# Performance work log

Measured on AMD Instinct MI355X. Metric: run time of the kernel, lower is better.

## Reference

```python
import jax, jax.numpy as jnp
import numpy as np

B, F_IN, D_IN = 1024, 64, 64
N_CAPS, D_CAPS = 32, 64
ROUTINGS = 3
HEADS = 2
EPS = 1e-7  # K.epsilon()


def setup_inputs() -> dict:
    key = jax.random.key(0)
    ks = jax.random.split(key, 8)
    P = N_CAPS * (N_CAPS - 1) // 2
    return {
        "x": jax.random.normal(ks[0], (B, F_IN, D_IN), jnp.float32),
        "reweight_W": jax.random.normal(ks[1], (D_IN, N_CAPS, D_CAPS), jnp.float32) * 0.05,
        "routing_init": 10.0 * jax.random.truncated_normal(ks[2], -2.0, 2.0, (N_CAPS, F_IN), jnp.float32),
        "kernel_fm": jnp.full((N_CAPS, 1), 0.5, jnp.float32),
        "bias_fm": jnp.zeros((D_CAPS,), jnp.float32),
        "kernel_mf": jnp.ones((P, 1), jnp.float32),
        "bias_mf": jnp.zeros((D_CAPS,), jnp.float32),
        "kernel_highint": jnp.full((N_CAPS, 1), 0.5, jnp.float32),
        "bias_highint": jnp.zeros((D_CAPS * HEADS,), jnp.float32),
        "W_query": jax.random.normal(ks[3], (D_CAPS, D_CAPS * HEADS), jnp.float32) * 0.05,
        "W_key": jax.random.normal(ks[4], (D_CAPS, D_CAPS * HEADS), jnp.float32) * 0.05,
        "W_value": jax.random.normal(ks[5], (D_CAPS, D_CAPS * HEADS), jnp.float32) * 0.05,
        "W_res": jax.random.normal(ks[6], (D_CAPS, D_CAPS * HEADS), jnp.float32) * 0.05,
    }


def _squash(v):
    s = jnp.sum(v * v, axis=-1, keepdims=True) + EPS
    return (jnp.sqrt(s) / (0.5 + s)) * v


def _heads(t):
    # [B,N,H*F] -> [H,B,N,F] (matches tf.stack(tf.split(t, H, axis=2)))
    b, n, _ = t.shape
    return t.reshape(b, n, HEADS, D_CAPS).transpose(2, 0, 1, 3)


def reference(x, reweight_W, routing_init, kernel_fm, bias_fm, kernel_mf, bias_mf,
              kernel_highint, bias_highint, W_query, W_key, W_value, W_res):
    # inputs_hat: [B, N, F, C]
    inputs_hat = jnp.einsum('bfd,dnc->bnfc', x, reweight_W)
    b_logits = jnp.broadcast_to(routing_init[None], (x.shape[0], N_CAPS, F_IN))
    for _ in range(ROUTINGS):
        c = jax.nn.softmax(b_logits, axis=1)            # softmax over capsules
        outputs = _squash(jnp.einsum('bnf,bnfc->bnc', c, inputs_hat))
        b_logits = b_logits + jnp.einsum('bnc,bnfc->bnf', outputs, inputs_hat)
    c = jax.nn.softmax(b_logits, axis=1)
    routing_score = c[..., None]                        # [B,N,F,1]
    attention_output = routing_score * inputs_hat       # [B,N,F,C]

    # FM per-field: square-of-sum minus sum-of-square over input capsules
    sum_f = jnp.sum(attention_output, axis=2)           # [B,N,C]
    field_fm = sum_f ** 2 - jnp.sum(attention_output ** 2, axis=2)
    hi_fm = jnp.sum(field_fm * kernel_fm[None], axis=1) + bias_fm  # [B,C]

    field_wise_vectors = sum_f                          # [B,N,C]

    # pairwise MF interactions (itertools.combinations order == triu indices)
    li, ri = np.triu_indices(N_CAPS, k=1)
    emb_prod = field_wise_vectors[:, li] * field_wise_vectors[:, ri]  # [B,P,C]
    h_mf = jnp.sum(emb_prod * kernel_mf[None], axis=1) + bias_mf      # [B,C]

    # InteractingLayer (multi-head self-attention over fields, use_res=True)
    q = _heads(jnp.einsum('bnd,de->bne', field_wise_vectors, W_query))  # [H,B,N,F]
    k = _heads(jnp.einsum('bnd,de->bne', field_wise_vectors, W_key))
    v = _heads(jnp.einsum('bnd,de->bne', field_wise_vectors, W_value))
    attn = jax.nn.softmax(jnp.einsum('hbnf,hbmf->hbnm', q, k), axis=-1)
    out = jnp.einsum('hbnm,hbmf->hbnf', attn, v)        # [H,B,N,F]
    out = out.transpose(1, 2, 0, 3).reshape(x.shape[0], N_CAPS, HEADS * D_CAPS)
    res = jnp.einsum('bnd,de->bne', field_wise_vectors, W_res)
    fv2 = jax.nn.relu(out + res)                        # [B,N,H*F]
    high_int = jnp.sum(fv2 * kernel_highint[None], axis=1) + bias_highint  # [B,2C]

    return jnp.concatenate([hi_fm, h_mf, high_int], axis=-1), routing_score
```

## Files before the change

### kernel.cpp

```cpp
#include <hip/hip_runtime.h>


#define EPS_SQ 1e-7f

typedef __attribute__((ext_vector_type(8))) short bf16x8;
typedef __attribute__((ext_vector_type(4))) float floatx4;

__device__ __forceinline__ int lidx(int r, int c) {
  return r * 68 + ((((c >> 2) ^ (r >> 2)) & 15) << 2) + (c & 3);
}
__device__ __forceinline__ int lidx64(int r, int c) {
  return r * 64 + ((((c >> 2) ^ r ^ (r >> 2)) & 15) << 2) + (c & 3);
}
__device__ __forceinline__ unsigned short f2bf(float f) {
  unsigned u = __float_as_uint(f);
  u += 0x7FFFu + ((u >> 16) & 1u);
  return (unsigned short)(u >> 16);
}

__global__ __launch_bounds__(256) void k_prep2(
    const float* __restrict__ W, const float* __restrict__ Wq,
    const float* __restrict__ Wk, const float* __restrict__ kmf,
    float* __restrict__ Qb, float* __restrict__ Ab, float* __restrict__ Kb,
    unsigned short* __restrict__ Wbf)
{
  const int t = threadIdx.x;
  if (blockIdx.x < 32) {
    __shared__ __align__(16) float Mn[64 * 68];
    const int n = blockIdx.x;
#pragma unroll
    for (int k = 0; k < 4; k++) {
      int lin = t + 256 * k; int d = lin >> 4; int c0 = (lin & 15) << 2;
      *(float4*)&Mn[lidx(d, c0)] = *(const float4*)(W + d * 2048 + n * 64 + c0);
    }
    __syncthreads();
    const int d1 = (t >> 4) * 4, d2 = (t & 15) * 4;
    float acc[4][4] = {};
    for (int cq = 0; cq < 64; cq += 4) {
      float m1[4][4], m2[4][4];
#pragma unroll
      for (int i = 0; i < 4; i++) *(float4*)m1[i] = *(const float4*)&Mn[lidx(d1 + i, cq)];
#pragma unroll
      for (int j = 0; j < 4; j++) *(float4*)m2[j] = *(const float4*)&Mn[lidx(d2 + j, cq)];
#pragma unroll
      for (int i = 0; i < 4; i++)
#pragma unroll
        for (int j = 0; j < 4; j++) {
          float s = 0.f;
#pragma unroll
          for (int k = 0; k < 4; k++) s += m1[i][k] * m2[j][k];
          acc[i][j] += s;
        }
    }
#pragma unroll
    for (int i = 0; i < 4; i++)
      *(float4*)(Qb + n * 4096 + (d1 + i) * 64 + d2) = *(float4*)acc[i];
  } else if (blockIdx.x < 40) {
    __shared__ __align__(16) float wkS[64 * 68];
    __shared__ __align__(16) float wqS[16 * 68];
    const int hb = blockIdx.x - 32;
    const int h = hb & 1, rg = hb >> 1;
#pragma unroll
    for (int k = 0; k < 4; k++) {
      int lin = t + 256 * k; int dp = lin >> 4; int e0 = (lin & 15) << 2;
      *(float4*)&wkS[lidx(dp, e0)] = *(const float4*)(Wk + dp * 128 + h * 64 + e0);
    }
    {
      int dl = t >> 4, e0 = (t & 15) << 2;
      *(float4*)&wqS[lidx(dl, e0)] = *(const float4*)(Wq + (rg * 16 + dl) * 128 + h * 64 + e0);
    }
    __syncthreads();
    const int dl = t >> 4, dp0 = (t & 15) << 2;
    float acc[4] = {};
    for (int e = 0; e < 64; e += 4) {
      float q4[4];
      *(float4*)q4 = *(const float4*)&wqS[lidx(dl, e)];
#pragma unroll
      for (int c = 0; c < 4; c++) {
        float mr[4];
        *(float4*)mr = *(const float4*)&wkS[lidx(dp0 + c, e)];
        acc[c] += q4[0] * mr[0] + q4[1] * mr[1] + q4[2] * mr[2] + q4[3] * mr[3];
      }
    }
    *(float4*)(Ab + h * 4096 + (rg * 16 + dl) * 64 + dp0) = *(float4*)acc;
  } else if (blockIdx.x == 40) {
    __shared__ float Ks[1024];
    *(float4*)&Ks[t * 4] = make_float4(0.f, 0.f, 0.f, 0.f);
    __syncthreads();
    if (t < 248) {
#pragma unroll
      for (int j = 0; j < 2; j++) {
        int p = t * 2 + j;
        if (p < 496) {
          int l = 0, rem = p;
          while (rem >= 31 - l) { rem -= 31 - l; ++l; }
          int r = l + 1 + rem;
          float v = kmf[p];
          Ks[l * 32 + r] = v;
          Ks[r * 32 + l] = v;
        }
      }
    }
    __syncthreads();
    *(float4*)&Kb[t * 4] = *(const float4*)&Ks[t * 4];
  } else {
    const int n = blockIdx.x - 41;
#pragma unroll
    for (int k = 0; k < 2; k++) {
      int lin = t + 256 * k;
      int c = lin >> 3, dg = lin & 7;
      unsigned short tmp[8];
#pragma unroll
      for (int dl = 0; dl < 8; dl++)
        tmp[dl] = f2bf(W[(dg * 8 + dl) * 2048 + n * 64 + c]);
      *(uint4*)&Wbf[n * 4096 + c * 64 + ((dg ^ (c & 7)) << 3)] = *(uint4*)tmp;
    }
  }
}

__global__ __launch_bounds__(512, 4) void k_route3(
    const float* __restrict__ x, const float* __restrict__ W,
    const float* __restrict__ rinit, const float* __restrict__ Qb,
    float* __restrict__ rs, float* __restrict__ fwv)
{
  __shared__ __align__(16) float smem[2 * 10240];

  const int t = threadIdx.x;
  const int tb = t >> 8, tt = t & 255;
  const int b = blockIdx.x * 2 + tb;

  float* xs  = smem + tb * 10240;
  float* bS  = smem + tb * 10240 + 4096;
  float* cOw = smem + tb * 10240 + 6144;
  float* xcS = smem + tb * 10240 + 8192;

  float* xc0 = smem + 8192;
  float* xc1 = smem + 10240 + 8192;
  float* ow0 = smem + 6144;
  float* ow1 = smem + 10240 + 6144;

#pragma unroll
  for (int k = 0; k < 4; k++) {
    int lin = tt + 256 * k; int f = lin >> 4; int d0 = (lin & 15) << 2;
    *(float4*)&xs[lidx64(f, d0)] = *(const float4*)(x + b * 4096 + f * 64 + d0);
  }
#pragma unroll
  for (int k = 0; k < 2; k++) {
    int lin = tt + 256 * k; int n = lin >> 4; int f0 = (lin & 15) << 2;
    *(float4*)&bS[lidx64(n, f0)] = *(const float4*)(rinit + n * 64 + f0);
  }
  __syncthreads();

  const int tn = tt >> 4, tlo = tt & 15;
  const int nq = t >> 4, sub = t & 15;

  for (int it = 0; it < 4; it++) {
    {
      const int nl = tt & 31, fg = tt >> 5;
#pragma unroll
      for (int qq = 0; qq < 2; qq++) {
        const int f0 = (fg * 2 + qq) * 4;
        float v[4];
        *(float4*)v = *(const float4*)&bS[lidx64(nl, f0)];
        float e[4];
#pragma unroll
        for (int j = 0; j < 4; j++) {
          float m = v[j];
          m = fmaxf(m, __shfl_xor(m, 16, 64));
          m = fmaxf(m, __shfl_xor(m, 8, 64));
          m = fmaxf(m, __shfl_xor(m, 4, 64));
          m = fmaxf(m, __shfl_xor(m, 2, 64));
          m = fmaxf(m, __shfl_xor(m, 1, 64));
          e[j] = __expf(v[j] - m);
          float s = e[j];
          s += __shfl_xor(s, 16, 64);
          s += __shfl_xor(s, 8, 64);
          s += __shfl_xor(s, 4, 64);
          s += __shfl_xor(s, 2, 64);
          s += __shfl_xor(s, 1, 64);
          e[j] /= s;
        }
        *(float4*)&cOw[lidx64(nl, f0)] = *(float4*)e;
      }
    }
    __syncthreads();
    if (it == 3) {
#pragma unroll
      for (int k = 0; k < 2; k++) {
        int lin = tt + 256 * k;
        int n = lin >> 4, fq = lin & 15;
        float4 v = *(const float4*)&cOw[lidx64(n, fq * 4)];
        *(float4*)(rs + b * 2048 + n * 64 + fq * 4) = v;
      }
    }
    {
      const int n0 = tn * 2, d0 = tlo * 4;
      float acc[2][4] = {{0, 0, 0, 0}, {0, 0, 0, 0}};
      for (int fq = 0; fq < 16; fq++) {
        float c0[4], c1[4];
        *(float4*)c0 = *(const float4*)&cOw[lidx64(n0, fq * 4)];
        *(float4*)c1 = *(const float4*)&cOw[lidx64(n0 + 1, fq * 4)];
#pragma unroll
        for (int j = 0; j < 4; j++) {
          float xr[4];
          *(float4*)xr = *(const float4*)&xs[lidx64(fq * 4 + j, d0)];
#pragma unroll
          for (int i = 0; i < 4; i++) {
            acc[0][i] += c0[j] * xr[i];
            acc[1][i] += c1[j] * xr[i];
          }
        }
      }
      *(float4*)&xcS[lidx64(n0, d0)] = *(float4*)acc[0];
      *(float4*)&xcS[lidx64(n0 + 1, d0)] = *(float4*)acc[1];
    }
    __syncthreads();
    if (it == 3) break;

    {
      const float* Qn = Qb + nq * 4096 + sub * 4;
      float y0[4] = {}, y1[4] = {};
#pragma unroll 4
      for (int dq = 0; dq < 16; dq++) {
        float xv0[4], xv1[4];
        *(float4*)xv0 = *(const float4*)&xc0[lidx64(nq, dq * 4)];
        *(float4*)xv1 = *(const float4*)&xc1[lidx64(nq, dq * 4)];
#pragma unroll
        for (int j = 0; j < 4; j++) {
          float4 q = *(const float4*)(Qn + (dq * 4 + j) * 64);
          y0[0] += xv0[j] * q.x; y0[1] += xv0[j] * q.y;
          y0[2] += xv0[j] * q.z; y0[3] += xv0[j] * q.w;
          y1[0] += xv1[j] * q.x; y1[1] += xv1[j] * q.y;
          y1[2] += xv1[j] * q.z; y1[3] += xv1[j] * q.w;
        }
      }
      float xa0[4], xa1[4];
      *(float4*)xa0 = *(const float4*)&xc0[lidx64(nq, sub * 4)];
      *(float4*)xa1 = *(const float4*)&xc1[lidx64(nq, sub * 4)];
      float ps0 = y0[0] * xa0[0] + y0[1] * xa0[1] + y0[2] * xa0[2] + y0[3] * xa0[3];
      float ps1 = y1[0] * xa1[0] + y1[1] * xa1[1] + y1[2] * xa1[2] + y1[3] * xa1[3];
      ps0 += __shfl_xor(ps0, 1, 64); ps0 += __shfl_xor(ps0, 2, 64);
      ps0 += __shfl_xor(ps0, 4, 64); ps0 += __shfl_xor(ps0, 8, 64);
      ps1 += __shfl_xor(ps1, 1, 64); ps1 += __shfl_xor(ps1, 2, 64);
      ps1 += __shfl_xor(ps1, 4, 64); ps1 += __shfl_xor(ps1, 8, 64);
      const float ss0 = ps0 + EPS_SQ, ss1 = ps1 + EPS_SQ;
      const float sc0 = sqrtf(ss0) / (0.5f + ss0);
      const float sc1 = sqrtf(ss1) / (0.5f + ss1);
      float o0[4] = {y0[0] * sc0, y0[1] * sc0, y0[2] * sc0, y0[3] * sc0};
      float o1[4] = {y1[0] * sc1, y1[1] * sc1, y1[2] * sc1, y1[3] * sc1};
      *(float4*)&ow0[lidx64(nq, sub * 4)] = *(float4*)o0;
      *(float4*)&ow1[lidx64(nq, sub * 4)] = *(float4*)o1;
    }
    __syncthreads();

    {
      const int n0 = tn * 2, f0 = tlo * 4;
      float acc[2][4] = {{0, 0, 0, 0}, {0, 0, 0, 0}};
      for (int dq = 0; dq < 64; dq += 4) {
        float o[2][4];
        *(float4*)o[0] = *(const float4*)&cOw[lidx64(n0, dq)];
        *(float4*)o[1] = *(const float4*)&cOw[lidx64(n0 + 1, dq)];
#pragma unroll
        for (int i = 0; i < 4; i++) {
          float xr[4];
          *(float4*)xr = *(const float4*)&xs[lidx64(f0 + i, dq)];
#pragma unroll
          for (int k = 0; k < 4; k++) {
            acc[0][i] += o[0][k] * xr[k];
            acc[1][i] += o[1][k] * xr[k];
          }
        }
      }
#pragma unroll
      for (int j = 0; j < 2; j++) {
        float tmp[4];
        *(float4*)tmp = *(const float4*)&bS[lidx64(n0 + j, f0)];
#pragma unroll
        for (int i = 0; i < 4; i++) tmp[i] += acc[j][i];
        *(float4*)&bS[lidx64(n0 + j, f0)] = *(float4*)tmp;
      }
    }
    __syncthreads();
  }

  {
    const float* Wn = W + nq * 64 + sub * 4;
    float a0[4] = {}, a1[4] = {};
#pragma unroll 4
    for (int dq = 0; dq < 16; dq++) {
      float xv0[4], xv1[4];
      *(float4*)xv0 = *(const float4*)&xc0[lidx64(nq, dq * 4)];
      *(float4*)xv1 = *(const float4*)&xc1[lidx64(nq, dq * 4)];
#pragma unroll
      for (int j = 0; j < 4; j++) {
        float4 w = *(const float4*)(Wn + (dq * 4 + j) * 2048);
        a0[0] += xv0[j] * w.x; a0[1] += xv0[j] * w.y;
        a0[2] += xv0[j] * w.z; a0[3] += xv0[j] * w.w;
        a1[0] += xv1[j] * w.x; a1[1] += xv1[j] * w.y;
        a1[2] += xv1[j] * w.z; a1[3] += xv1[j] * w.w;
      }
    }
    const int b0g = blockIdx.x * 2;
    *(float4*)(fwv + b0g * 2048 + nq * 64 + sub * 4) = *(float4*)a0;
    *(float4*)(fwv + (b0g + 1) * 2048 + nq * 64 + sub * 4) = *(float4*)a1;
  }
}

__global__ __launch_bounds__(256) void k_ih(
    const float* __restrict__ x, const unsigned short* __restrict__ Wbf,
    const float* __restrict__ rs, float* __restrict__ ssq)
{
  __shared__ __align__(16) unsigned short xB[4 * 64 * 64];
  __shared__ unsigned short cF2[4 * 8 * 64];
  const int n_oct = (blockIdx.x & 3) << 3, b0 = (blockIdx.x >> 2) * 4;
  const int t = threadIdx.x, w = t >> 6, lane = t & 63;

#pragma unroll
  for (int k = 0; k < 16; k++) {
    int ch = t + 256 * k;
    int bb = ch >> 10, rem = ch & 1023;
    int f = rem >> 4, fq = rem & 15;
    int dg = fq >> 1, half = fq & 1;
    float4 v = *(const float4*)(x + ((b0 + bb) * 64 + f) * 64 + fq * 4);
    unsigned p0 = f2bf(v.x) | ((unsigned)f2bf(v.y) << 16);
    unsigned p1 = f2bf(v.z) | ((unsigned)f2bf(v.w) << 16);
    *(uint2*)&xB[bb * 4096 + f * 64 + ((dg ^ (f & 7)) << 3) + half * 4] =
        make_uint2(p0, p1);
  }
#pragma unroll
  for (int nn = 0; nn < 8; nn++) {
    float v = rs[(b0 + w) * 2048 + (n_oct + nn) * 64 + lane];
    cF2[(w * 8 + nn) * 64 + lane] = f2bf(v * v);
  }
  __syncthreads();

  const int m = lane & 15, q = lane >> 4, ms = m & 7;
  bf16x8 a[4][2];
#pragma unroll
  for (int mi = 0; mi < 4; mi++) {
    const unsigned short* bp = xB + w * 4096 + (mi * 16 + m) * 64;
#pragma unroll
    for (int kk = 0; kk < 2; kk++)
      a[mi][kk] = *(const bf16x8*)&bp[((kk * 4 + q) ^ ms) << 3];
  }

  for (int np = 0; np < 4; np++) {
    const int n0 = n_oct + np * 2;
#pragma unroll
    for (int nn = 0; nn < 2; nn++) {
      bf16x8 bf[4][2];
#pragma unroll
      for (int ci = 0; ci < 4; ci++) {
        const unsigned short* bp = Wbf + (n0 + nn) * 4096 + (ci * 16 + m) * 64;
#pragma unroll
        for (int kk = 0; kk < 2; kk++)
          bf[ci][kk] = *(const bf16x8*)&bp[((kk * 4 + q) ^ ms) << 3];
      }
      float ps[4] = {0.f, 0.f, 0.f, 0.f};
      const unsigned short* cf = cF2 + (w * 8 + np * 2 + nn) * 64 + q * 4;
#pragma unroll
      for (int mi = 0; mi < 4; mi++) {
        float cfv[4];
#pragma unroll
        for (int r = 0; r < 4; r++)
          cfv[r] = __uint_as_float((unsigned)cf[mi * 16 + r] << 16);
#pragma unroll
        for (int ci = 0; ci < 4; ci++) {
          floatx4 c0 = {0.f, 0.f, 0.f, 0.f};
          c0 = __builtin_amdgcn_mfma_f32_16x16x32_bf16(a[mi][0], bf[ci][0], c0, 0, 0, 0);
          c0 = __builtin_amdgcn_mfma_f32_16x16x32_bf16(a[mi][1], bf[ci][1], c0, 0, 0, 0);
#pragma unroll
          for (int r = 0; r < 4; r++) { float tv = c0[r]; ps[ci] += cfv[r] * tv * tv; }
        }
      }
#pragma unroll
      for (int ci = 0; ci < 4; ci++) {
        ps[ci] += __shfl_xor(ps[ci], 16, 64);
        ps[ci] += __shfl_xor(ps[ci], 32, 64);
      }
      if (q == 0) {
#pragma unroll
        for (int ci = 0; ci < 4; ci++)
          ssq[(b0 + w) * 2048 + (n0 + nn) * 64 + ci * 16 + m] = ps[ci];
      }
    }
  }
}

__global__ __launch_bounds__(256) void k_attn(
    const float* __restrict__ fwv, const float* __restrict__ ssq,
    const float* __restrict__ Ab, const float* __restrict__ Kb,
    const float* __restrict__ Wv, const float* __restrict__ Wr,
    const float* __restrict__ kfm, const float* __restrict__ bfm,
    const float* __restrict__ bmf, const float* __restrict__ khi,
    const float* __restrict__ bhi, float* __restrict__ out0)
{
  __shared__ __align__(16) float smem[8832];
  float* fwS  = smem;
  float* pS   = smem + 2176;
  float* bufA = smem + 4480;
  float* tS   = smem + 6656;
  float* vS   = smem + 4480;
  float* redH = smem + 2176;
  float* Kf   = smem + 4480;
  float* red1 = smem + 5536;

  const int b = blockIdx.x, t = threadIdx.x;
  const int tn = t >> 4, te = t & 15;
  const int n0 = tn * 2, e0 = te * 8, d0 = te * 4;

#pragma unroll
  for (int k = 0; k < 2; k++) {
    int lin = t + 256 * k; int nn = lin >> 4; int c0 = (lin & 15) << 2;
    *(float4*)&fwS[lidx(nn, c0)] = *(const float4*)(fwv + b * 2048 + nn * 64 + c0);
  }
  __syncthreads();

  for (int h = 0; h < 2; h++) {
    float tacc[2][4] = {};
    for (int half = 0; half < 2; half++) {
#pragma unroll
      for (int k = 0; k < 2; k++) {
        int lin = t + 256 * k; int d = lin >> 4; int c0 = (lin & 15) << 2;
        *(float4*)&bufA[lidx(d, c0)] =
            *(const float4*)(Ab + h * 4096 + (half * 32 + d) * 64 + c0);
      }
      __syncthreads();
      for (int dq = 0; dq < 32; dq += 4) {
        float fw0[4], fw1[4];
        *(float4*)fw0 = *(const float4*)&fwS[lidx(n0, half * 32 + dq)];
        *(float4*)fw1 = *(const float4*)&fwS[lidx(n0 + 1, half * 32 + dq)];
#pragma unroll
        for (int j = 0; j < 4; j++) {
          float mr[4];
          *(float4*)mr = *(const float4*)&bufA[lidx(dq + j, d0)];
#pragma unroll
          for (int c = 0; c < 4; c++) {
            tacc[0][c] += fw0[j] * mr[c];
            tacc[1][c] += fw1[j] * mr[c];
          }
        }
      }
      __syncthreads();
    }
    *(float4*)&tS[lidx(n0, d0)] = *(float4*)tacc[0];
    *(float4*)&tS[lidx(n0 + 1, d0)] = *(float4*)tacc[1];
    __syncthreads();
    {
      const int m0 = te * 2;
      float s00 = 0.f, s01 = 0.f, s10 = 0.f, s11 = 0.f;
      for (int kk = 0; kk < 16; kk++) {
        float ta0[4], ta1[4], f0[4], f1[4];
        *(float4*)ta0 = *(const float4*)&tS[lidx(n0, kk * 4)];
        *(float4*)ta1 = *(const float4*)&tS[lidx(n0 + 1, kk * 4)];
        *(float4*)f0 = *(const float4*)&fwS[lidx(m0, kk * 4)];
        *(float4*)f1 = *(const float4*)&fwS[lidx(m0 + 1, kk * 4)];
#pragma unroll
        for (int j = 0; j < 4; j++) {
          s00 += ta0[j] * f0[j]; s01 += ta0[j] * f1[j];
          s10 += ta1[j] * f0[j]; s11 += ta1[j] * f1[j];
        }
      }
      pS[(h * 32 + n0) * 36 + m0] = s00;
      pS[(h * 32 + n0) * 36 + m0 + 1] = s01;
      pS[(h * 32 + n0 + 1) * 36 + m0] = s10;
      pS[(h * 32 + n0 + 1) * 36 + m0 + 1] = s11;
    }
    __syncthreads();
  }

  {
    const int r = t >> 2, sub = t & 3;
    const int base = r * 36 + sub * 8;
    float v0[4], v1[4];
    *(float4*)v0 = *(const float4*)&pS[base];
    *(float4*)v1 = *(const float4*)&pS[base + 4];
    float mx = fmaxf(fmaxf(fmaxf(v0[0], v0[1]), fmaxf(v0[2], v0[3])),
                     fmaxf(fmaxf(v1[0], v1[1]), fmaxf(v1[2], v1[3])));
    mx = fmaxf(mx, __shfl_xor(mx, 1, 64));
    mx = fmaxf(mx, __shfl_xor(mx, 2, 64));
    float sum = 0.f;
#pragma unroll
    for (int j = 0; j < 4; j++) { v0[j] = __expf(v0[j] - mx); sum += v0[j]; }
#pragma unroll
    for (int j = 0; j < 4; j++) { v1[j] = __expf(v1[j] - mx); sum += v1[j]; }
    sum += __shfl_xor(sum, 1, 64);
    sum += __shfl_xor(sum, 2, 64);
    const float inv = 1.0f / sum;
#pragma unroll
    for (int j = 0; j < 4; j++) { v0[j] *= inv; v1[j] *= inv; }
    *(float4*)&pS[base] = *(float4*)v0;
    *(float4*)&pS[base + 4] = *(float4*)v1;
  }
  __syncthreads();

  {
    float acc[2][8] = {};
    for (int dq = 0; dq < 64; dq += 4) {
      float fw0[4], fw1[4];
      *(float4*)fw0 = *(const float4*)&fwS[lidx(n0, dq)];
      *(float4*)fw1 = *(const float4*)&fwS[lidx(n0 + 1, dq)];
#pragma unroll
      for (int jj = 0; jj < 4; jj++) {
        float w8[8];
        *(float4*)&w8[0] = *(const float4*)(Wv + (dq + jj) * 128 + e0);
        *(float4*)&w8[4] = *(const float4*)(Wv + (dq + jj) * 128 + e0 + 4);
#pragma unroll
        for (int j = 0; j < 8; j++) {
          acc[0][j] += fw0[jj] * w8[j];
          acc[1][j] += fw1[jj] * w8[j];
        }
      }
    }
    *(float4*)&vS[n0 * 132 + e0] = *(float4*)&acc[0][0];
    *(float4*)&vS[n0 * 132 + e0 + 4] = *(float4*)&acc[0][4];
    *(float4*)&vS[(n0 + 1) * 132 + e0] = *(float4*)&acc[1][0];
    *(float4*)&vS[(n0 + 1) * 132 + e0 + 4] = *(float4*)&acc[1][4];
  }
  __syncthreads();

  {
    const int h2 = te >> 3;
    float pacc[2][8] = {};
    for (int m4 = 0; m4 < 8; m4++) {
      float p0v[4], p1v[4];
      *(float4*)p0v = *(const float4*)&pS[(h2 * 32 + n0) * 36 + m4 * 4];
      *(float4*)p1v = *(const float4*)&pS[(h2 * 32 + n0 + 1) * 36 + m4 * 4];
#pragma unroll
      for (int mm = 0; mm < 4; mm++) {
        const int m = m4 * 4 + mm;
        float vr[8];
        *(float4*)&vr[0] = *(const float4*)&vS[m * 132 + e0];
        *(float4*)&vr[4] = *(const float4*)&vS[m * 132 + e0 + 4];
#pragma unroll
        for (int j = 0; j < 8; j++) {
          pacc[0][j] += p0v[mm] * vr[j];
          pacc[1][j] += p1v[mm] * vr[j];
        }
      }
    }
    for (int dq = 0; dq < 64; dq += 4) {
      float fw0[4], fw1[4];
      *(float4*)fw0 = *(const float4*)&fwS[lidx(n0, dq)];
      *(float4*)fw1 = *(const float4*)&fwS[lidx(n0 + 1, dq)];
#pragma unroll
      for (int jj = 0; jj < 4; jj++) {
        float w8[8];
        *(float4*)&w8[0] = *(const float4*)(Wr + (dq + jj) * 128 + e0);
        *(float4*)&w8[4] = *(const float4*)(Wr + (dq + jj) * 128 + e0 + 4);
#pragma unroll
        for (int j = 0; j < 8; j++) {
          pacc[0][j] += fw0[jj] * w8[j];
          pacc[1][j] += fw1[jj] * w8[j];
        }
      }
    }
    __syncthreads();
    {
      float kh0 = khi[n0], kh1 = khi[n0 + 1];
      float ph[8];
#pragma unroll
      for (int j = 0; j < 8; j++)
        ph[j] = kh0 * fmaxf(pacc[0][j], 0.f) + kh1 * fmaxf(pacc[1][j], 0.f);
      *(float4*)&redH[tn * 132 + e0] = *(float4*)&ph[0];
      *(float4*)&redH[tn * 132 + e0 + 4] = *(float4*)&ph[4];
    }
  }
  {
    const int p4 = t * 4;
    float4 kv = *(const float4*)(Kb + p4);
    const int n = p4 >> 5, r = p4 & 31;
    Kf[n * 33 + r]     = kv.x;
    Kf[n * 33 + r + 1] = kv.y;
    Kf[n * 33 + r + 2] = kv.z;
    Kf[n * 33 + r + 3] = kv.w;
  }
  __syncthreads();

  {
    float acc[2][4] = {{0, 0, 0, 0}, {0, 0, 0, 0}};
    for (int r = 0; r < 32; r++) {
      const float k0 = Kf[n0 * 33 + r];
      const float k1 = Kf[(n0 + 1) * 33 + r];
      float fr[4];
      *(float4*)fr = *(const float4*)&fwS[lidx(r, d0)];
#pragma unroll
      for (int i = 0; i < 4; i++) {
        acc[0][i] += k0 * fr[i];
        acc[1][i] += k1 * fr[i];
      }
    }
    *(float4*)&tS[lidx(n0, d0)] = *(float4*)acc[0];
    *(float4*)&tS[lidx(n0 + 1, d0)] = *(float4*)acc[1];
  }
  __syncthreads();

  if (t < 128) {
    float s = 0.f;
#pragma unroll
    for (int k = 0; k < 16; k++) s += redH[k * 132 + t];
    out0[b * 256 + 128 + t] = s + bhi[t];
  }
  {
    const int c = t & 63, nq = t >> 6;
    float p = 0.f;
#pragma unroll
    for (int k = 0; k < 8; k++) {
      int nn = nq * 8 + k;
      float fv = fwS[lidx(nn, c)];
      float sv = ssq[b * 2048 + nn * 64 + c];
      p += (fv * fv - sv) * kfm[nn];
    }
    red1[nq * 68 + c] = p;
    float hmf = 0.f;
#pragma unroll
    for (int l8 = 0; l8 < 8; l8++) {
      const int l = nq * 8 + l8;
      hmf += fwS[lidx(l, c)] * tS[lidx(l, c)];
    }
    red1[(4 + nq) * 68 + c] = hmf;
  }
  __syncthreads();
  if (t < 64) {
    out0[b * 256 + t] = red1[t] + red1[68 + t] + red1[136 + t] + red1[204 + t] + bfm[t];
    float h2 = red1[272 + t] + red1[340 + t] + red1[408 + t] + red1[476 + t];
    out0[b * 256 + 64 + t] = 0.5f * h2 + bmf[t];
  }
}

extern "C" void kernel_launch(void* const* d_in, const int* in_sizes, int n_in,
                              void* d_out, int out_size, void* d_ws, size_t ws_size,
                              hipStream_t stream) {
  (void)in_sizes; (void)n_in; (void)out_size; (void)ws_size;
  const float* x     = (const float*)d_in[0];
  const float* W     = (const float*)d_in[1];
  const float* rinit = (const float*)d_in[2];
  const float* kfm   = (const float*)d_in[3];
  const float* bfm   = (const float*)d_in[4];
  const float* kmf   = (const float*)d_in[5];
  const float* bmf   = (const float*)d_in[6];
  const float* khi   = (const float*)d_in[7];
  const float* bhi   = (const float*)d_in[8];
  const float* Wq    = (const float*)d_in[9];
  const float* Wk    = (const float*)d_in[10];
  const float* Wv    = (const float*)d_in[11];
  const float* Wr    = (const float*)d_in[12];

  float* out0 = (float*)d_out;
  float* rs   = out0 + 1024 * 256;

  float* ws   = (float*)d_ws;
  float* Abuf = ws;
  float* Kbuf = ws + 8192;
  float* Qbuf = ws + 16384;
  unsigned short* Wbf = (unsigned short*)(ws + 262144);
  float* fwv  = ws + 2097152;
  float* ssq  = ws + 2 * 2097152;

  k_prep2<<<73, 256, 0, stream>>>(W, Wq, Wk, kmf, Qbuf, Abuf, Kbuf, Wbf);
  k_route3<<<512, 512, 0, stream>>>(x, W, rinit, Qbuf, rs, fwv);
  k_ih<<<1024, 256, 0, stream>>>(x, Wbf, rs, ssq);
  k_attn<<<1024, 256, 0, stream>>>(fwv, ssq, Abuf, Kbuf, Wv, Wr,
                                   kfm, bfm, bmf, khi, bhi, out0);
}
```

Baseline: 252.2 us.

## Fuse squared-sum MFMA kernel into attention kernel, drop ssq buffer

```diff
diff --git a/kernel.cpp b/kernel.cpp
--- a/kernel.cpp
+++ b/kernel.cpp
@@ -306,89 +306,9 @@
   }
 }
 
-__global__ __launch_bounds__(256) void k_ih(
-    const float* __restrict__ x, const unsigned short* __restrict__ Wbf,
-    const float* __restrict__ rs, float* __restrict__ ssq)
-{
-  __shared__ __align__(16) unsigned short xB[4 * 64 * 64];
-  __shared__ unsigned short cF2[4 * 8 * 64];
-  const int n_oct = (blockIdx.x & 3) << 3, b0 = (blockIdx.x >> 2) * 4;
-  const int t = threadIdx.x, w = t >> 6, lane = t & 63;
-
-#pragma unroll
-  for (int k = 0; k < 16; k++) {
-    int ch = t + 256 * k;
-    int bb = ch >> 10, rem = ch & 1023;
-    int f = rem >> 4, fq = rem & 15;
-    int dg = fq >> 1, half = fq & 1;
-    float4 v = *(const float4*)(x + ((b0 + bb) * 64 + f) * 64 + fq * 4);
-    unsigned p0 = f2bf(v.x) | ((unsigned)f2bf(v.y) << 16);
-    unsigned p1 = f2bf(v.z) | ((unsigned)f2bf(v.w) << 16);
-    *(uint2*)&xB[bb * 4096 + f * 64 + ((dg ^ (f & 7)) << 3) + half * 4] =
-        make_uint2(p0, p1);
-  }
-#pragma unroll
-  for (int nn = 0; nn < 8; nn++) {
-    float v = rs[(b0 + w) * 2048 + (n_oct + nn) * 64 + lane];
-    cF2[(w * 8 + nn) * 64 + lane] = f2bf(v * v);
-  }
-  __syncthreads();
-
-  const int m = lane & 15, q = lane >> 4, ms = m & 7;
-  bf16x8 a[4][2];
-#pragma unroll
-  for (int mi = 0; mi < 4; mi++) {
-    const unsigned short* bp = xB + w * 4096 + (mi * 16 + m) * 64;
-#pragma unroll
-    for (int kk = 0; kk < 2; kk++)
-      a[mi][kk] = *(const bf16x8*)&bp[((kk * 4 + q) ^ ms) << 3];
-  }
-
-  for (int np = 0; np < 4; np++) {
-    const int n0 = n_oct + np * 2;
-#pragma unroll
-    for (int nn = 0; nn < 2; nn++) {
-      bf16x8 bf[4][2];
-#pragma unroll
-      for (int ci = 0; ci < 4; ci++) {
-        const unsigned short* bp = Wbf + (n0 + nn) * 4096 + (ci * 16 + m) * 64;
-#pragma unroll
-        for (int kk = 0; kk < 2; kk++)
-          bf[ci][kk] = *(const bf16x8*)&bp[((kk * 4 + q) ^ ms) << 3];
-      }
-      float ps[4] = {0.f, 0.f, 0.f, 0.f};
-      const unsigned short* cf = cF2 + (w * 8 + np * 2 + nn) * 64 + q * 4;
-#pragma unroll
-      for (int mi = 0; mi < 4; mi++) {
-        float cfv[4];
-#pragma unroll
-        for (int r = 0; r < 4; r++)
-          cfv[r] = __uint_as_float((unsigned)cf[mi * 16 + r] << 16);
-#pragma unroll
-        for (int ci = 0; ci < 4; ci++) {
-          floatx4 c0 = {0.f, 0.f, 0.f, 0.f};
-          c0 = __builtin_amdgcn_mfma_f32_16x16x32_bf16(a[mi][0], bf[ci][0], c0, 0, 0, 0);
-          c0 = __builtin_amdgcn_mfma_f32_16x16x32_bf16(a[mi][1], bf[ci][1], c0, 0, 0, 0);
-#pragma unroll
-          for (int r = 0; r < 4; r++) { float tv = c0[r]; ps[ci] += cfv[r] * tv * tv; }
-        }
-      }
-#pragma unroll
-      for (int ci = 0; ci < 4; ci++) {
-        ps[ci] += __shfl_xor(ps[ci], 16, 64);
-        ps[ci] += __shfl_xor(ps[ci], 32, 64);
-      }
-      if (q == 0) {
-#pragma unroll
-        for (int ci = 0; ci < 4; ci++)
-          ssq[(b0 + w) * 2048 + (n0 + nn) * 64 + ci * 16 + m] = ps[ci];
-      }
-    }
-  }
-}
-
-__global__ __launch_bounds__(256) void k_attn(
-    const float* __restrict__ fwv, const float* __restrict__ ssq,
+__global__ __launch_bounds__(256, 4) void k_attn2(
+    const float* __restrict__ fwv, const float* __restrict__ x,
+    const unsigned short* __restrict__ Wbf, const float* __restrict__ rs,
     const float* __restrict__ Ab, const float* __restrict__ Kb,
     const float* __restrict__ Wv, const float* __restrict__ Wr,
     const float* __restrict__ kfm, const float* __restrict__ bfm,
@@ -404,15 +324,103 @@
   float* redH = smem + 2176;
   float* Kf   = smem + 4480;
   float* red1 = smem + 5536;
+  unsigned short* xB   = (unsigned short*)(smem + 2176);
+  unsigned short* cF2s = (unsigned short*)(smem + 4480);
+  float*          ssqS = smem + 6656;
 
   const int b = blockIdx.x, t = threadIdx.x;
   const int tn = t >> 4, te = t & 15;
   const int n0 = tn * 2, e0 = te * 8, d0 = te * 4;
+  const int w = t >> 6, lane = t & 63;
 
 #pragma unroll
   for (int k = 0; k < 2; k++) {
     int lin = t + 256 * k; int nn = lin >> 4; int c0 = (lin & 15) << 2;
     *(float4*)&fwS[lidx(nn, c0)] = *(const float4*)(fwv + b * 2048 + nn * 64 + c0);
+  }
+#pragma unroll
+  for (int k = 0; k < 4; k++) {
+    int ch = t + 256 * k;
+    int f = ch >> 4, fq = ch & 15;
+    int dg = fq >> 1, half = fq & 1;
+    float4 v = *(const float4*)(x + (b * 64 + f) * 64 + fq * 4);
+    unsigned p0 = f2bf(v.x) | ((unsigned)f2bf(v.y) << 16);
+    unsigned p1 = f2bf(v.z) | ((unsigned)f2bf(v.w) << 16);
+    *(uint2*)&xB[f * 64 + ((dg ^ (f & 7)) << 3) + half * 4] = make_uint2(p0, p1);
+  }
+#pragma unroll
+  for (int k = 0; k < 2; k++) {
+    int lin = t + 256 * k;
+    int n = lin >> 4, f0 = (lin & 15) << 2;
+    float4 v = *(const float4*)(rs + b * 2048 + n * 64 + f0);
+    unsigned short t4[4] = {f2bf(v.x * v.x), f2bf(v.y * v.y),
+                            f2bf(v.z * v.z), f2bf(v.w * v.w)};
+    *(uint2*)&cF2s[n * 64 + f0] = *(uint2*)t4;
+  }
+  __syncthreads();
+
+  {
+    const int m = lane & 15, q = lane >> 4, ms = m & 7;
+    bf16x8 a_[4][2];
+#pragma unroll
+    for (int mi = 0; mi < 4; mi++) {
+      const unsigned short* bp = xB + (mi * 16 + m) * 64;
+#pragma unroll
+      for (int kk = 0; kk < 2; kk++)
+        a_[mi][kk] = *(const bf16x8*)&bp[((kk * 4 + q) ^ ms) << 3];
+    }
+#pragma unroll 2
+    for (int nn = 0; nn < 8; nn++) {
+      const int n = w * 8 + nn;
+      bf16x8 bf[4][2];
+#pragma unroll
+      for (int ci = 0; ci < 4; ci++) {
+        const unsigned short* bp = Wbf + n * 4096 + (ci * 16 + m) * 64;
+#pragma unroll
+        for (int kk = 0; kk < 2; kk++)
+          bf[ci][kk] = *(const bf16x8*)&bp[((kk * 4 + q) ^ ms) << 3];
+      }
+      float ps[4] = {0.f, 0.f, 0.f, 0.f};
+      const unsigned short* cf = cF2s + n * 64 + q * 4;
+#pragma unroll
+      for (int mi = 0; mi < 4; mi++) {
+        float cfv[4];
+#pragma unroll
+        for (int r = 0; r < 4; r++)
+          cfv[r] = __uint_as_float((unsigned)cf[mi * 16 + r] << 16);
+#pragma unroll
+        for (int ci = 0; ci < 4; ci++) {
+          floatx4 c0 = {0.f, 0.f, 0.f, 0.f};
+          c0 = __builtin_amdgcn_mfma_f32_16x16x32_bf16(a_[mi][0], bf[ci][0], c0, 0, 0, 0);
+          c0 = __builtin_amdgcn_mfma_f32_16x16x32_bf16(a_[mi][1], bf[ci][1], c0, 0, 0, 0);
+#pragma unroll
+          for (int r = 0; r < 4; r++) { float tv = c0[r]; ps[ci] += cfv[r] * tv * tv; }
+        }
+      }
+#pragma unroll
+      for (int ci = 0; ci < 4; ci++) {
+        ps[ci] += __shfl_xor(ps[ci], 16, 64);
+        ps[ci] += __shfl_xor(ps[ci], 32, 64);
+      }
+      if (q == 0) {
+#pragma unroll
+        for (int ci = 0; ci < 4; ci++)
+          ssqS[n * 64 + ci * 16 + m] = ps[ci];
+      }
+    }
+  }
+  __syncthreads();
+
+  float p_reg = 0.f;
+  {
+    const int c = t & 63, nqf = t >> 6;
+#pragma unroll
+    for (int k = 0; k < 8; k++) {
+      int nn = nqf * 8 + k;
+      float fv = fwS[lidx(nn, c)];
+      float sv = ssqS[nn * 64 + c];
+      p_reg += (fv * fv - sv) * kfm[nn];
+    }
   }
   __syncthreads();
 
@@ -603,15 +611,7 @@
   }
   {
     const int c = t & 63, nq = t >> 6;
-    float p = 0.f;
-#pragma unroll
-    for (int k = 0; k < 8; k++) {
-      int nn = nq * 8 + k;
-      float fv = fwS[lidx(nn, c)];
-      float sv = ssq[b * 2048 + nn * 64 + c];
-      p += (fv * fv - sv) * kfm[nn];
-    }
-    red1[nq * 68 + c] = p;
+    red1[nq * 68 + c] = p_reg;
     float hmf = 0.f;
 #pragma unroll
     for (int l8 = 0; l8 < 8; l8++) {
@@ -655,11 +655,9 @@
   float* Qbuf = ws + 16384;
   unsigned short* Wbf = (unsigned short*)(ws + 262144);
   float* fwv  = ws + 2097152;
-  float* ssq  = ws + 2 * 2097152;
 
   k_prep2<<<73, 256, 0, stream>>>(W, Wq, Wk, kmf, Qbuf, Abuf, Kbuf, Wbf);
   k_route3<<<512, 512, 0, stream>>>(x, W, rinit, Qbuf, rs, fwv);
-  k_ih<<<1024, 256, 0, stream>>>(x, Wbf, rs, ssq);
-  k_attn<<<1024, 256, 0, stream>>>(fwv, ssq, Abuf, Kbuf, Wv, Wr,
-                                   kfm, bfm, bmf, khi, bhi, out0);
+  k_attn2<<<1024, 256, 0, stream>>>(fwv, x, Wbf, rs, Abuf, Kbuf, Wv, Wr,
+                                    kfm, bfm, bmf, khi, bhi, out0);
 }
```

Result: slower. 264.6 us (+4.9%).
